# Kernel tuning notes

Measured on AMD Instinct MI355X. Metric: run time of the kernel, lower is better.

Reference implementation:

```python
import jax, jax.numpy as jnp
import numpy as np


def _decode_and_scale(boxes_cxcywh, orig_target_sizes):
    # cxcywh -> xyxy, then scale by [w, h, w, h] per image
    cx, cy, w, h = jnp.split(boxes_cxcywh, 4, axis=-1)  # each [B, Q, 1]
    xyxy = jnp.concatenate([cx - 0.5 * w, cy - 0.5 * h, cx + 0.5 * w, cy + 0.5 * h], axis=-1)
    scale = jnp.tile(orig_target_sizes, (1, 2))[:, None, :]  # [B, 1, 4]
    return xyxy * scale


def setup_inputs() -> dict:
    key = jax.random.key(0)
    k1, k2, k3 = jax.random.split(key, 3)
    B, Q, C = 256, 1000, 80
    return {
        "pred_logits": jax.random.normal(k1, (B, Q, C), dtype=jnp.float32),
        "pred_boxes": jax.random.uniform(k2, (B, Q, 4), dtype=jnp.float32),
        "orig_target_sizes": jax.random.uniform(k3, (B, 2), dtype=jnp.float32),
        "num_top_queries": 300,
    }


def reference(pred_logits, pred_boxes, orig_target_sizes, num_top_queries):
    B, Q, C = pred_logits.shape
    bbox_pred = _decode_and_scale(pred_boxes, orig_target_sizes)  # [B, Q, 4]
    # focal-loss path: sigmoid, flattened top-k over queries*classes
    scores = jax.nn.sigmoid(pred_logits).reshape(B, Q * C)
    top_scores, index = jax.lax.top_k(scores, num_top_queries)  # [B, K]
    labels = index % C
    query_index = index // C
    final_boxes = jnp.take_along_axis(bbox_pred, query_index[..., None], axis=1)  # [B, K, 4]
    return labels, final_boxes, top_scores
```

## Files before the change

kernel.cpp:

```cpp
#include <hip/hip_runtime.h>


constexpr int   NT    = 1024;
constexpr int   NBINS = 4096;
constexpr int   CAPL  = 4096;
constexpr float THR   = 2.4f;

__device__ __forceinline__ unsigned f2key(float f) {
    unsigned u = __float_as_uint(f);
    return (u & 0x80000000u) ? ~u : (u | 0x80000000u);
}
__device__ __forceinline__ float key2f(unsigned k) {
    unsigned u = (k & 0x80000000u) ? (k & 0x7FFFFFFFu) : ~k;
    return __uint_as_float(u);
}
__device__ __forceinline__ unsigned long long packkv(unsigned key, unsigned idx) {
    return ((unsigned long long)key << 32) | (unsigned long long)(0xFFFFFFFFu - idx);
}

__device__ __forceinline__ void consume1(
    float x, unsigned idx, unsigned* lcnt, unsigned long long* cand)
{
    if (x > THR) {
        unsigned p = atomicAdd(lcnt, 1u);
        if (p < (unsigned)CAPL) cand[p] = packkv(f2key(x), idx);
    }
}
__device__ __forceinline__ void consume4(
    float4 v, int i4, int N4, unsigned* lcnt, unsigned long long* cand)
{
    if (i4 < N4) {
        float mx = fmaxf(fmaxf(v.x, v.y), fmaxf(v.z, v.w));
        if (mx > THR) {
            unsigned bi = (unsigned)(4 * i4);
            consume1(v.x, bi + 0, lcnt, cand);
            consume1(v.y, bi + 1, lcnt, cand);
            consume1(v.z, bi + 2, lcnt, cand);
            consume1(v.w, bi + 3, lcnt, cand);
        }
    }
}

__global__ __launch_bounds__(NT, 4) void dfine_fused_kernel(
    const float* __restrict__ logits,
    const float* __restrict__ pboxes,
    const float* __restrict__ sizes,
    float* __restrict__ out,
    int B, int Q, int C, int K)
{
    const int b   = blockIdx.x;
    const int tid = threadIdx.x;
    const int N   = Q * C;
    const int N4  = N >> 2;
    const float4* __restrict__ base4 = reinterpret_cast<const float4*>(logits + (long long)b * N);

    __shared__ unsigned long long cand[CAPL];
    __shared__ unsigned hist[NBINS];
    __shared__ unsigned partial[NT];
    __shared__ unsigned lcnt;
    __shared__ unsigned candCount;
    __shared__ unsigned threshBin;

    if (tid == 0) lcnt = 0u;
    __syncthreads();

    {
        float4 va[7], vb[7], vc[6];
        #pragma unroll
        for (int j = 0; j < 7; ++j) {
            int i4 = j * NT + tid;
            va[j] = base4[(i4 < N4) ? i4 : (N4 - 1)];
        }
        __builtin_amdgcn_sched_barrier(0);
        #pragma unroll
        for (int j = 0; j < 7; ++j) {
            int i4 = (7 + j) * NT + tid;
            vb[j] = base4[(i4 < N4) ? i4 : (N4 - 1)];
        }
        __builtin_amdgcn_sched_barrier(0);
        #pragma unroll
        for (int j = 0; j < 7; ++j)
            consume4(va[j], j * NT + tid, N4, &lcnt, cand);
        __builtin_amdgcn_sched_barrier(0);
        #pragma unroll
        for (int j = 0; j < 6; ++j) {
            int i4 = (14 + j) * NT + tid;
            vc[j] = base4[(i4 < N4) ? i4 : (N4 - 1)];
        }
        __builtin_amdgcn_sched_barrier(0);
        #pragma unroll
        for (int j = 0; j < 7; ++j)
            consume4(vb[j], (7 + j) * NT + tid, N4, &lcnt, cand);
        __builtin_amdgcn_sched_barrier(0);
        #pragma unroll
        for (int j = 0; j < 6; ++j)
            consume4(vc[j], (14 + j) * NT + tid, N4, &lcnt, cand);
    }
    for (int i4 = 20 * NT + tid; i4 < N4; i4 += NT)
        consume4(base4[i4], i4, N4, &lcnt, cand);
    __syncthreads();

    int n;
    const unsigned tot = lcnt;
    if (tot >= (unsigned)K && tot <= (unsigned)CAPL) {
        n = (int)tot;
    } else {
        const float* __restrict__ lg = logits + (long long)b * N;
        for (int i = tid; i < NBINS; i += NT) hist[i] = 0u;
        if (tid == 0) candCount = 0u;
        __syncthreads();
        for (int i = tid; i < N; i += NT)
            atomicAdd(&hist[f2key(lg[i]) >> 20], 1u);
        __syncthreads();
        {
            const int BPT = NBINS / NT;
            unsigned s = 0;
            #pragma unroll
            for (int m = 0; m < BPT; ++m) s += hist[tid * BPT + m];
            partial[tid] = s;
        }
        __syncthreads();
        if (tid < 64) {
            const int PPG = NT / 64;
            unsigned gs = 0;
            #pragma unroll
            for (int m = 0; m < PPG; ++m) gs += partial[tid * PPG + m];
            unsigned pre = gs;
            #pragma unroll
            for (int off = 1; off < 64; off <<= 1) {
                unsigned t = __shfl_up(pre, off);
                if (tid >= off) pre += t;
            }
            unsigned total = __shfl(pre, 63);
            unsigned suf   = total - (pre - gs);
            unsigned long long m1 = __ballot(suf >= (unsigned)K);
            int g = 63 - __clzll(m1);
            unsigned above = total - __shfl(pre, g);
            unsigned hv = hist[g * 64 + tid];
            unsigned pre2 = hv;
            #pragma unroll
            for (int off = 1; off < 64; off <<= 1) {
                unsigned t = __shfl_up(pre2, off);
                if (tid >= off) pre2 += t;
            }
            unsigned total2 = __shfl(pre2, 63);
            unsigned suf2   = above + total2 - (pre2 - hv);
            unsigned long long m2 = __ballot(suf2 >= (unsigned)K);
            int l2 = 63 - __clzll(m2);
            if (tid == 0) threshBin = (unsigned)(g * 64 + l2);
        }
        __syncthreads();
        const unsigned tb = threshBin;
        for (int i = tid; i < N; i += NT) {
            unsigned k = f2key(lg[i]);
            if ((k >> 20) >= tb) {
                unsigned p = atomicAdd(&candCount, 1u);
                if (p < (unsigned)CAPL) cand[p] = packkv(k, (unsigned)i);
            }
        }
        __syncthreads();
        n = (int)min(candCount, (unsigned)CAPL);
    }

    const int BK = B * K;
    float* __restrict__ out_labels = out;
    float* __restrict__ out_boxes  = out + BK;
    float* __restrict__ out_scores = out + (long long)BK * 5;
    const float s0 = sizes[2 * b];
    const float s1 = sizes[2 * b + 1];

    for (int t = tid; t < n; t += NT) {
        unsigned long long my = cand[t];
        int r = 0;
        for (int j = 0; j < n; ++j) r += (cand[j] > my);
        if (r < K) {
            unsigned key = (unsigned)(my >> 32);
            unsigned idx = 0xFFFFFFFFu - (unsigned)(my & 0xFFFFFFFFull);
            float logit = key2f(key);
            float score = 1.0f / (1.0f + expf(-logit));
            int label = (int)(idx % (unsigned)C);
            int q     = (int)(idx / (unsigned)C);
            float4 bp = *reinterpret_cast<const float4*>(pboxes + ((long long)b * Q + q) * 4);
            int o = b * K + r;
            out_labels[o] = (float)label;
            out_scores[o] = score;
            float4 bb;
            bb.x = (bp.x - 0.5f * bp.z) * s0;
            bb.y = (bp.y - 0.5f * bp.w) * s1;
            bb.z = (bp.x + 0.5f * bp.z) * s0;
            bb.w = (bp.y + 0.5f * bp.w) * s1;
            *reinterpret_cast<float4*>(out_boxes + 4LL * o) = bb;
        }
    }
}

extern "C" void kernel_launch(void* const* d_in, const int* in_sizes, int n_in,
                              void* d_out, int out_size, void* d_ws, size_t ws_size,
                              hipStream_t stream) {
    const float* logits = (const float*)d_in[0];
    const float* pboxes = (const float*)d_in[1];
    const float* sizes  = (const float*)d_in[2];

    const int B = in_sizes[2] / 2;
    const int Q = in_sizes[1] / (4 * B);
    const int C = in_sizes[0] / (B * Q);
    const int K = out_size / (6 * B);

    dfine_fused_kernel<<<B, NT, 0, stream>>>(
        logits, pboxes, sizes, (float*)d_out, B, Q, C, K);
}
```

Measured before the change: 36.07 us.

## Stream logits through triple-buffered LDS via global_load_lds async copies

Replaces the register-staged float4 loads with direct global-to-LDS DMA loads (global_load_lds), using three 32KB chunk buffers and vmcnt waits so each wave consumes its own slice while later chunks are in flight. The histogram and partial arrays now alias the DMA buffers in the fallback path. The threshold rises from 2.4 to 2.5, which shrinks the candidate set and the O(n^2) rank pass but makes the histogram fallback more likely if fewer than K values exceed it. The large LDS footprint (about 100KB) limits the kernel to one block per CU, trading occupancy for explicit asynchronous prefetch.

```diff
diff --git a/kernel.cpp b/kernel.cpp
--- a/kernel.cpp
+++ b/kernel.cpp
@@ -1,10 +1,13 @@
 #include <hip/hip_runtime.h>
-
-
-constexpr int   NT    = 1024;
-constexpr int   NBINS = 4096;
-constexpr int   CAPL  = 4096;
-constexpr float THR   = 2.4f;
+#include <cstdint>
+
+
+constexpr int   NT     = 1024;
+constexpr int   NBINS  = 4096;
+constexpr int   CAPL   = 4096;
+constexpr int   CHUNK4 = 2048;
+constexpr int   NBUF   = 3;
+constexpr float THR    = 2.5f;
 
 __device__ __forceinline__ unsigned f2key(float f) {
     unsigned u = __float_as_uint(f);
@@ -16,6 +19,12 @@
 }
 __device__ __forceinline__ unsigned long long packkv(unsigned key, unsigned idx) {
     return ((unsigned long long)key << 32) | (unsigned long long)(0xFFFFFFFFu - idx);
+}
+
+typedef const __attribute__((address_space(1))) unsigned g_u32;
+typedef __attribute__((address_space(3))) unsigned l_u32;
+__device__ __forceinline__ void gload_lds16(const void* g, void* l) {
+    __builtin_amdgcn_global_load_lds((g_u32*)g, (l_u32*)l, 16, 0, 0);
 }
 
 __device__ __forceinline__ void consume1(
@@ -41,7 +50,7 @@
     }
 }
 
-__global__ __launch_bounds__(NT, 4) void dfine_fused_kernel(
+__global__ __launch_bounds__(NT) void dfine_fused_kernel(
     const float* __restrict__ logits,
     const float* __restrict__ pboxes,
     const float* __restrict__ sizes,
@@ -50,13 +59,14 @@
 {
     const int b   = blockIdx.x;
     const int tid = threadIdx.x;
+    const int w   = tid >> 6;
+    const int l   = tid & 63;
     const int N   = Q * C;
     const int N4  = N >> 2;
     const float4* __restrict__ base4 = reinterpret_cast<const float4*>(logits + (long long)b * N);
 
+    __shared__ alignas(16) char dmabuf[NBUF][CHUNK4 * 16];
     __shared__ unsigned long long cand[CAPL];
-    __shared__ unsigned hist[NBINS];
-    __shared__ unsigned partial[NT];
     __shared__ unsigned lcnt;
     __shared__ unsigned candCount;
     __shared__ unsigned threshBin;
@@ -65,39 +75,37 @@
     __syncthreads();
 
     {
-        float4 va[7], vb[7], vc[6];
-        #pragma unroll
-        for (int j = 0; j < 7; ++j) {
-            int i4 = j * NT + tid;
-            va[j] = base4[(i4 < N4) ? i4 : (N4 - 1)];
-        }
+        const int NCH = (N4 + CHUNK4 - 1) / CHUNK4;
+
+        auto issue = [&](int c) {
+            if (c >= NCH) return;
+            char* lb = &dmabuf[c % NBUF][(w * 128) * 16];
+            int bi4 = c * CHUNK4 + w * 128;
+            #pragma unroll
+            for (int inst = 0; inst < 2; ++inst) {
+                int i4 = bi4 + inst * 64 + l;
+                gload_lds16(base4 + ((i4 < N4) ? i4 : (N4 - 1)), lb + inst * 1024);
+            }
+        };
+
+        issue(0); issue(1); issue(2);
         __builtin_amdgcn_sched_barrier(0);
-        #pragma unroll
-        for (int j = 0; j < 7; ++j) {
-            int i4 = (7 + j) * NT + tid;
-            vb[j] = base4[(i4 < N4) ? i4 : (N4 - 1)];
-        }
-        __builtin_amdgcn_sched_barrier(0);
-        #pragma unroll
-        for (int j = 0; j < 7; ++j)
-            consume4(va[j], j * NT + tid, N4, &lcnt, cand);
-        __builtin_amdgcn_sched_barrier(0);
-        #pragma unroll
-        for (int j = 0; j < 6; ++j) {
-            int i4 = (14 + j) * NT + tid;
-            vc[j] = base4[(i4 < N4) ? i4 : (N4 - 1)];
-        }
-        __builtin_amdgcn_sched_barrier(0);
-        #pragma unroll
-        for (int j = 0; j < 7; ++j)
-            consume4(vb[j], (7 + j) * NT + tid, N4, &lcnt, cand);
-        __builtin_amdgcn_sched_barrier(0);
-        #pragma unroll
-        for (int j = 0; j < 6; ++j)
-            consume4(vc[j], (14 + j) * NT + tid, N4, &lcnt, cand);
-    }
-    for (int i4 = 20 * NT + tid; i4 < N4; i4 += NT)
-        consume4(base4[i4], i4, N4, &lcnt, cand);
+        for (int c = 0; c < NCH; ++c) {
+            if (c + 2 < NCH)      asm volatile("s_waitcnt vmcnt(4)" ::: "memory");
+            else if (c + 1 < NCH) asm volatile("s_waitcnt vmcnt(2)" ::: "memory");
+            else                  asm volatile("s_waitcnt vmcnt(0)" ::: "memory");
+            __builtin_amdgcn_sched_barrier(0);
+            const char* lb = &dmabuf[c % NBUF][(w * 128) * 16];
+            float4 v0 = *reinterpret_cast<const float4*>(lb + l * 16);
+            float4 v1 = *reinterpret_cast<const float4*>(lb + (64 + l) * 16);
+            int i40 = c * CHUNK4 + w * 128 + l;
+            consume4(v0, i40,      N4, &lcnt, cand);
+            consume4(v1, i40 + 64, N4, &lcnt, cand);
+            __builtin_amdgcn_sched_barrier(0);
+            issue(c + 3);
+            __builtin_amdgcn_sched_barrier(0);
+        }
+    }
     __syncthreads();
 
     int n;
@@ -105,6 +113,8 @@
     if (tot >= (unsigned)K && tot <= (unsigned)CAPL) {
         n = (int)tot;
     } else {
+        unsigned* hist    = reinterpret_cast<unsigned*>(&dmabuf[0][0]);
+        unsigned* partial = hist + NBINS;
         const float* __restrict__ lg = logits + (long long)b * N;
         for (int i = tid; i < NBINS; i += NT) hist[i] = 0u;
         if (tid == 0) candCount = 0u;
```

Measured after the change: 30.60 us. -15.2%, faster.
